# Performance work log

Measured on AMD Instinct MI355X. Metric: run time of the kernel, lower is better.

The kernel has to match this reference:

```python
import jax, jax.numpy as jnp
import numpy as np

KH = KW = 3  # deform conv kernel
EPS = 1e-12  # F.normalize eps


def _deform_sample(img, u, v):
    """Flow-guided deformable sampling: bilinear gather of img at each of the
    9 kernel offsets shifted by the per-pixel flow (u=dx, v=dy).
    img: [B,C,H,W]; u,v: [B,1,H,W] -> returns [B,C,9,H,W]."""
    B, C, H, W = img.shape
    ky, kx = jnp.meshgrid(jnp.arange(KH) - 1, jnp.arange(KW) - 1, indexing='ij')
    ky = ky.reshape(1, 9, 1, 1).astype(img.dtype)
    kx = kx.reshape(1, 9, 1, 1).astype(img.dtype)
    iy = jnp.arange(H, dtype=img.dtype).reshape(1, 1, H, 1)
    ix = jnp.arange(W, dtype=img.dtype).reshape(1, 1, 1, W)
    py = iy + ky + v  # [B,9,H,W]
    px = ix + kx + u
    y0 = jnp.floor(py); x0 = jnp.floor(px)
    wy = py - y0; wx = px - x0  # bilinear weights
    y0i = y0.astype(jnp.int32); x0i = x0.astype(jnp.int32)
    flat = img.reshape(B, C, H * W)

    def gather(yi, xi):
        valid = ((yi >= 0) & (yi < H) & (xi >= 0) & (xi < W)).astype(img.dtype)
        idx = jnp.clip(yi, 0, H - 1) * W + jnp.clip(xi, 0, W - 1)  # [B,9,H,W]
        g = jax.vmap(lambda f, i: jnp.take(f, i.reshape(-1), axis=1))(flat, idx)
        return g.reshape(B, C, 9, H, W) * valid[:, None]

    s = (gather(y0i, x0i) * ((1 - wy) * (1 - wx))[:, None]
         + gather(y0i, x0i + 1) * ((1 - wy) * wx)[:, None]
         + gather(y0i + 1, x0i) * (wy * (1 - wx))[:, None]
         + gather(y0i + 1, x0i + 1) * (wy * wx)[:, None])
    return s


def setup_inputs() -> dict:
    key = jax.random.key(0)
    k1, k2, k3, k4, k5 = jax.random.split(key, 5)
    B, C, H, W = 2, 64, 256, 256
    num_heads = 4
    clone = jax.random.normal(k1, (B, C, H, W), dtype=jnp.float32)
    x = jax.random.normal(k2, (B, C, H * W), dtype=jnp.float32)
    u = jax.random.normal(k3, (B, 1, H, W), dtype=jnp.float32)
    v = jax.random.normal(k4, (B, 1, H, W), dtype=jnp.float32)
    weight = jax.random.normal(k5, (C, C, KH, KW), dtype=jnp.float32) * 0.05
    temperature = jnp.ones((num_heads, 1, 1), dtype=jnp.float32)
    return {"clone": clone, "x": x, "u": u, "v": v,
            "weight": weight, "temperature": temperature}


def reference(clone, x, u, v, weight, temperature):
    # deformable conv: bilinear gather then contract over (in_ch, kernel)
    s = _deform_sample(clone, u, v)                      # [B,C,9,H,W]
    w = weight.reshape(weight.shape[0], weight.shape[1], 9)
    conv = jnp.einsum('bckhw,ock->bohw', s, w)           # [B,C,H,W]
    B, C, H, W = conv.shape
    head = temperature.shape[0]
    kv = conv.reshape(B, head, C // head, H * W)          # k = v = deform output
    q = x.reshape(B, head, C // head, H * W)
    qn = q / jnp.maximum(jnp.linalg.norm(q, axis=-1, keepdims=True), EPS)
    kn = kv / jnp.maximum(jnp.linalg.norm(kv, axis=-1, keepdims=True), EPS)
    attn = jnp.einsum('bhcs,bhds->bhcd', qn, kn) * temperature  # [B,h,c,c]
    attn = jax.nn.softmax(attn, axis=-1)
    out = jnp.einsum('bhcd,bhds->bhcs', attn, kv)
    return out.reshape(B, C, H * W)
```

## Files before the change

### kernel.cpp

```cpp
#include <hip/hip_runtime.h>

typedef __bf16 bf16;
typedef __bf16 bf16x4 __attribute__((ext_vector_type(4)));
typedef __bf16 bf16x8 __attribute__((ext_vector_type(8)));
typedef float  f32x2  __attribute__((ext_vector_type(2)));
typedef float  f32x4  __attribute__((ext_vector_type(4)));
typedef float  f32x16 __attribute__((ext_vector_type(16)));

#define HH 256
#define WW 256
#define NB 2
#define NC 64
#define NS 65536
#define EX 258
#define NHEAD 4
#define DH 16
#define NSTRIPE 8
#define ACCSZ 2304

#define OFF_CEXT   0ul
#define OFF_KV     17040384ul
#define OFF_WPK    33817600ul
#define OFF_ACC    33891328ul

__global__ void k0w(const float* __restrict__ wgt, bf16* __restrict__ wpk,
                    float* __restrict__ accums) {
    int t = blockIdx.x * 256 + threadIdx.x;
    if (t < 9 * 2 * 4 * 64) {
        int L   = t & 63;
        int mtg = (t >> 6) & 3;
        int kc  = (t >> 8) & 1;
        int tap = t >> 9;
        int o  = mtg * 16 + (L & 15);
        int cb = kc * 32 + (L >> 4) * 8;
        bf16x8 vv;
        #pragma unroll
        for (int j = 0; j < 8; j++)
            vv[j] = (bf16)wgt[(o * 64 + (cb + j)) * 9 + tap];
        *(bf16x8*)(wpk + t * 8) = vv;
    }
    int z = t - 9 * 2 * 4 * 64;
    if (z >= 0 && z < NSTRIPE * ACCSZ) accums[z] = 0.0f;
}

__global__ __launch_bounds__(256, 2) void k1_conv(const float* __restrict__ clone,
                                                  const bf16* __restrict__ wpk,
                                                  bf16* __restrict__ cext) {
    const int Xt = blockIdx.x;
    const int Yt = blockIdx.y;
    const int b  = blockIdx.z;
    const int t  = threadIdx.x;
    const int L  = t & 63;
    const int wv = t >> 6;
    const int mpair = wv >> 1;
    const int npair = wv & 1;

    extern __shared__ bf16 tile[];

    bf16x8 afrag[2][9][2];
    #pragma unroll
    for (int mt = 0; mt < 2; mt++)
        #pragma unroll
        for (int tap = 0; tap < 9; tap++)
            #pragma unroll
            for (int kc = 0; kc < 2; kc++) {
                int idx = ((tap * 2 + kc) * 4 + (mpair * 2 + mt)) * 64 + L;
                afrag[mt][tap][kc] = *(const bf16x8*)(wpk + idx * 8);
            }

    for (int u = t; u < 2176; u += 256) {
        int xq = u % 17;
        int rc = u / 17;
        int cg = rc & 15;
        int r  = rc >> 4;
        int y  = Yt * 6 - 2 + r;
        int xg0 = Xt * 64 - 4 + xq * 4;
        int c0 = cg * 4;
        f32x4 f[4];
        bool yin = (y >= 0) && (y < HH);
        if (yin && xg0 >= 0 && xg0 + 3 < WW) {
            #pragma unroll
            for (int i = 0; i < 4; i++)
                f[i] = *(const f32x4*)(clone + ((size_t)(b * NC + c0 + i) * HH + y) * WW + xg0);
        } else {
            #pragma unroll
            for (int i = 0; i < 4; i++)
                #pragma unroll
                for (int e = 0; e < 4; e++) {
                    int xg = xg0 + e;
                    f[i][e] = (yin && xg >= 0 && xg < WW)
                            ? clone[((size_t)(b * NC + c0 + i) * HH + y) * WW + xg] : 0.0f;
                }
        }
        #pragma unroll
        for (int e = 0; e < 4; e++) {
            bf16x4 h;
            #pragma unroll
            for (int i = 0; i < 4; i++) h[i] = (bf16)f[i][e];
            *(bf16x4*)(tile + (r * 68 + xq * 4 + e) * 72 + c0) = h;
        }
    }
    __syncthreads();

    const int nbase = Xt * 64 + npair * 32;
    const f32x4 zero4 = {0.0f, 0.0f, 0.0f, 0.0f};
    for (int Yi = 0; Yi < 6; Yi++) {
        f32x4 acc[2][2];
        acc[0][0] = zero4; acc[0][1] = zero4; acc[1][0] = zero4; acc[1][1] = zero4;
        #pragma unroll
        for (int tap = 0; tap < 9; tap++) {
            const int ky = tap / 3 - 1;
            const int kx = tap % 3 - 1;
            const int r = Yi + 1 + ky;
            #pragma unroll
            for (int kc = 0; kc < 2; kc++) {
                const int cb = kc * 32 + (L >> 4) * 8;
                #pragma unroll
                for (int nt = 0; nt < 2; nt++) {
                    if (nbase + nt * 16 < EX) {
                        const int col = npair * 32 + nt * 16 + (L & 15) + kx + 3;
                        bf16x8 bfrag = *(const bf16x8*)(tile + (r * 68 + col) * 72 + cb);
                        #pragma unroll
                        for (int mt = 0; mt < 2; mt++)
                            acc[mt][nt] = __builtin_amdgcn_mfma_f32_16x16x32_bf16(
                                afrag[mt][tap][kc], bfrag, acc[mt][nt], 0, 0, 0);
                    }
                }
            }
        }
        int Yp = Yt * 6 + Yi;
        #pragma unroll
        for (int mt = 0; mt < 2; mt++)
            #pragma unroll
            for (int nt = 0; nt < 2; nt++) {
                int Xp = Xt * 64 + npair * 32 + nt * 16 + (L & 15);
                if (Xp < EX) {
                    int o = mpair * 32 + mt * 16 + (L >> 4) * 4;
                    bf16x4 st;
                    #pragma unroll
                    for (int rg = 0; rg < 4; rg++) st[rg] = (bf16)acc[mt][nt][rg];
                    *(bf16x4*)(cext + ((((size_t)b * EX + Yp) * EX + Xp) << 6) + o) = st;
                }
            }
    }
}

__global__ __launch_bounds__(256) void k2_gd(const float* __restrict__ uu,
                                             const float* __restrict__ vv,
                                             const float* __restrict__ x,
                                             const bf16* __restrict__ cext,
                                             bf16* __restrict__ kvT,
                                             float* __restrict__ accums) {
    const int bx = blockIdx.x;
    const int b  = blockIdx.z;
    const int strip = (bx & 7) * 128 + (bx >> 3);
    const int t = threadIdx.x;
    const int px = t >> 2;
    const int q4 = t & 3;
    const int hw = strip * 64 + px;
    const int idx = b * NS + hw;
    const int hy = hw >> 8;
    const int wx = hw & 255;

    __shared__ bf16 tile[64][68];

    float fv = vv[idx];
    float fu = uu[idx];
    float py_f = (float)hy + fv;
    float px_f = (float)wx + fu;
    float fy = floorf(py_f);
    float fx = floorf(px_f);
    float ay = py_f - fy;
    float ax = px_f - fx;
    int ys = (int)fy + 1;
    int xs = (int)fx + 1;
    float w00 = (1.0f - ay) * (1.0f - ax);
    float w01 = (1.0f - ay) * ax;
    float w10 = ay * (1.0f - ax);
    float w11 = ay * ax;
    bool y0i = (ys >= 0) && (ys < EX);
    bool y1i = (ys + 1 >= 0) && (ys + 1 < EX);
    bool x0i = (xs >= 0) && (xs < EX);
    bool x1i = (xs + 1 >= 0) && (xs + 1 < EX);
    if (!y0i) { w00 = 0.0f; w01 = 0.0f; }
    if (!y1i) { w10 = 0.0f; w11 = 0.0f; }
    if (!x0i) { w00 = 0.0f; w10 = 0.0f; }
    if (!x1i) { w01 = 0.0f; w11 = 0.0f; }
    int y0c = ys < 0 ? 0 : (ys > EX - 1 ? EX - 1 : ys);
    int y1c = ys + 1 < 0 ? 0 : (ys + 1 > EX - 1 ? EX - 1 : ys + 1);
    int x0c = xs < 0 ? 0 : (xs > EX - 1 ? EX - 1 : xs);
    int x1c = xs + 1 < 0 ? 0 : (xs + 1 > EX - 1 ? EX - 1 : xs + 1);
    const bf16* pb = cext + (((size_t)b * EX * EX) << 6);
    size_t i00 = ((size_t)(y0c * EX + x0c)) << 6;
    size_t i01 = ((size_t)(y0c * EX + x1c)) << 6;
    size_t i10 = ((size_t)(y1c * EX + x0c)) << 6;
    size_t i11 = ((size_t)(y1c * EX + x1c)) << 6;
    const int c0 = q4 * 16;
    bf16* kvp = kvT + ((size_t)(b * NS + hw)) * 64 + c0;
    #pragma unroll
    for (int g = 0; g < 2; g++) {
        int cg = c0 + g * 8;
        bf16x8 c00 = *(const bf16x8*)(pb + i00 + cg);
        bf16x8 c01 = *(const bf16x8*)(pb + i01 + cg);
        bf16x8 c10 = *(const bf16x8*)(pb + i10 + cg);
        bf16x8 c11 = *(const bf16x8*)(pb + i11 + cg);
        bf16x4 lo, hi;
        bf16x8 sv;
        #pragma unroll
        for (int j = 0; j < 8; j++) {
            float val = w00 * (float)c00[j] + w01 * (float)c01[j]
                      + w10 * (float)c10[j] + w11 * (float)c11[j];
            bf16 hv = (bf16)val;
            sv[j] = hv;
            if (j < 4) lo[j] = hv; else hi[j - 4] = hv;
        }
        *(bf16x8*)(kvp + g * 8) = sv;
        *(bf16x4*)(&tile[px][cg])     = lo;
        *(bf16x4*)(&tile[px][cg + 4]) = hi;
    }
    __syncthreads();

    const int L  = t & 63;
    const int h  = t >> 6;
    const int row = L & 15;
    const int kg  = L >> 4;
    const int bh = b * NHEAD + h;
    const float* qb = x + ((size_t)(b * NC + h * DH + row)) * NS + strip * 64;
    f32x4 acc = {0.0f, 0.0f, 0.0f, 0.0f};
    float qp = 0.0f, kp = 0.0f;
    #pragma unroll
    for (int it = 0; it < 2; it++) {
        const int s = it * 32 + kg * 8;
        f32x4 q0 = *(const f32x4*)(qb + s);
        f32x4 q1 = *(const f32x4*)(qb + s + 4);
        bf16x8 qa, ka;
        #pragma unroll
        for (int j = 0; j < 4; j++) {
            qa[j]     = (bf16)q0[j];
            qa[j + 4] = (bf16)q1[j];
        }
        #pragma unroll
        for (int j = 0; j < 8; j++) ka[j] = tile[s + j][h * DH + row];
        qp += q0[0]*q0[0] + q0[1]*q0[1] + q0[2]*q0[2] + q0[3]*q0[3]
            + q1[0]*q1[0] + q1[1]*q1[1] + q1[2]*q1[2] + q1[3]*q1[3];
        #pragma unroll
        for (int j = 0; j < 8; j++) {
            float kf = (float)ka[j];
            kp += kf * kf;
        }
        acc = __builtin_amdgcn_mfma_f32_16x16x32_bf16(qa, ka, acc, 0, 0, 0);
    }
    float* astripe = accums + (bx & 7) * ACCSZ;
    #pragma unroll
    for (int rg = 0; rg < 4; rg++)
        atomicAdd(astripe + bh * 256 + (kg * 4 + rg) * 16 + row, acc[rg]);
    qp += __shfl_xor(qp, 16); qp += __shfl_xor(qp, 32);
    kp += __shfl_xor(kp, 16); kp += __shfl_xor(kp, 32);
    if (kg == 0) {
        atomicAdd(astripe + 2048 + bh * 16 + row, qp);
        atomicAdd(astripe + 2176 + bh * 16 + row, kp);
    }
}

__global__ __launch_bounds__(256) void k5_out(const bf16* __restrict__ kvT,
                                              const float* __restrict__ accums,
                                              const float* __restrict__ temp,
                                              float* __restrict__ out) {
    const int bx = blockIdx.x;
    const int ci = (bx & 7) * 16 + (bx >> 3);
    const int h  = blockIdx.y;
    const int b  = blockIdx.z;
    const int t  = threadIdx.x;
    const int bh = b * NHEAD + h;
    __shared__ float l[256];
    __shared__ float a[256];
    {
        int i = t >> 4, j = t & 15;
        float dsum = 0.0f, q2 = 0.0f, k2 = 0.0f;
        #pragma unroll
        for (int st = 0; st < NSTRIPE; st++) {
            dsum += accums[st * ACCSZ + bh * 256 + t];
            q2   += accums[st * ACCSZ + 2048 + bh * 16 + i];
            k2   += accums[st * ACCSZ + 2176 + bh * 16 + j];
        }
        float qn = fmaxf(sqrtf(q2), 1e-12f);
        float kn = fmaxf(sqrtf(k2), 1e-12f);
        float logit = dsum / (qn * kn) * temp[h];
        l[t] = logit;
        __syncthreads();
        float mx = -1e30f;
        #pragma unroll
        for (int jj = 0; jj < 16; jj++) mx = fmaxf(mx, l[i * 16 + jj]);
        float sum = 0.0f;
        #pragma unroll
        for (int jj = 0; jj < 16; jj++) sum += expf(l[i * 16 + jj] - mx);
        a[t] = expf(logit - mx) / sum;
        __syncthreads();
    }

    const int L   = t & 63;
    const int wv  = t >> 6;
    const int r31 = L & 31;
    const int h5  = L >> 5;

    bf16x8 af;
    #pragma unroll
    for (int j = 0; j < 8; j++) {
        if (r31 < 16) {
            af[j] = (bf16)a[r31 * 16 + h5 * 8 + j];
        } else {
            float v  = a[(r31 - 16) * 16 + h5 * 8 + j];
            bf16 hv = (bf16)v;
            af[j] = (bf16)(v - (float)hv);
        }
    }

    const bf16* kvb = kvT + ((size_t)b * NS) * 64 + h * DH + h5 * 8;
    #pragma unroll
    for (int ch = 0; ch < 4; ch++) {
        const int s0 = ci * 512 + wv * 128 + ch * 32;
        bf16x8 kb = *(const bf16x8*)(kvb + (size_t)(s0 + r31) * 64);
        f32x16 acc;
        #pragma unroll
        for (int z = 0; z < 16; z++) acc[z] = 0.0f;
        acc = __builtin_amdgcn_mfma_f32_32x32x16_bf16(af, kb, acc, 0, 0, 0);
        #pragma unroll
        for (int reg = 0; reg < 8; reg++) {
            const int orow = (reg & 3) + 8 * (reg >> 2) + 4 * h5;
            out[(((size_t)(b * NC + h * DH + orow)) << 16) + s0 + r31]
                = acc[reg] + acc[reg + 8];
        }
    }
}

extern "C" void kernel_launch(void* const* d_in, const int* in_sizes, int n_in,
                              void* d_out, int out_size, void* d_ws, size_t ws_size,
                              hipStream_t stream) {
    const float* clone = (const float*)d_in[0];
    const float* x     = (const float*)d_in[1];
    const float* u     = (const float*)d_in[2];
    const float* v     = (const float*)d_in[3];
    const float* wgt   = (const float*)d_in[4];
    const float* temp  = (const float*)d_in[5];
    float* out = (float*)d_out;

    char* ws = (char*)d_ws;
    bf16*  cext   = (bf16*) (ws + OFF_CEXT);
    bf16*  kvT    = (bf16*) (ws + OFF_KV);
    bf16*  wpk    = (bf16*) (ws + OFF_WPK);
    float* accums = (float*)(ws + OFF_ACC);

    static bool attr_set = false;
    if (!attr_set) {
        hipFuncSetAttribute((const void*)k1_conv,
                            hipFuncAttributeMaxDynamicSharedMemorySize, 78336);
        attr_set = true;
    }

    k0w<<<90, 256, 0, stream>>>(wgt, wpk, accums);
    k1_conv<<<dim3(5, 43, 2), 256, 78336, stream>>>(clone, wpk, cext);
    k2_gd<<<dim3(1024, 1, 2), 256, 0, stream>>>(u, v, x, cext, kvT, accums);
    k5_out<<<dim3(128, 4, 2), 256, 0, stream>>>(kvT, accums, temp, out);
}
```

Before: 156.6 us.

## Stage conv-output window in shared memory for deformable gather

The gather kernel now processes 32-pixel strips and first loads a 9x40-pixel, 64-channel window of the conv output into LDS cooperatively. Bilinear corner reads are then served from LDS, with a fallback to global memory when the flow displaces a sample outside the window. This targets scattered, redundant global reads of neighbouring pixels. In exchange it adds about 46KB of LDS per block, doubles the grid with half the MFMA work per block, and issues twice as many accumulator atomics.

```diff
diff --git a/kernel.cpp b/kernel.cpp
--- a/kernel.cpp
+++ b/kernel.cpp
@@ -145,6 +145,8 @@
     }
 }
 
+#define WR 9
+#define WC 40
 __global__ __launch_bounds__(256) void k2_gd(const float* __restrict__ uu,
                                              const float* __restrict__ vv,
                                              const float* __restrict__ x,
@@ -153,57 +155,75 @@
                                              float* __restrict__ accums) {
     const int bx = blockIdx.x;
     const int b  = blockIdx.z;
-    const int strip = (bx & 7) * 128 + (bx >> 3);
+    const int strip = (bx & 7) * 256 + (bx >> 3);
     const int t = threadIdx.x;
-    const int px = t >> 2;
-    const int q4 = t & 3;
-    const int hw = strip * 64 + px;
-    const int idx = b * NS + hw;
-    const int hy = hw >> 8;
-    const int wx = hw & 255;
-
-    __shared__ bf16 tile[64][68];
-
-    float fv = vv[idx];
-    float fu = uu[idx];
-    float py_f = (float)hy + fv;
-    float px_f = (float)wx + fu;
-    float fy = floorf(py_f);
-    float fx = floorf(px_f);
-    float ay = py_f - fy;
-    float ax = px_f - fx;
-    int ys = (int)fy + 1;
-    int xs = (int)fx + 1;
-    float w00 = (1.0f - ay) * (1.0f - ax);
-    float w01 = (1.0f - ay) * ax;
-    float w10 = ay * (1.0f - ax);
-    float w11 = ay * ax;
-    bool y0i = (ys >= 0) && (ys < EX);
-    bool y1i = (ys + 1 >= 0) && (ys + 1 < EX);
-    bool x0i = (xs >= 0) && (xs < EX);
-    bool x1i = (xs + 1 >= 0) && (xs + 1 < EX);
-    if (!y0i) { w00 = 0.0f; w01 = 0.0f; }
-    if (!y1i) { w10 = 0.0f; w11 = 0.0f; }
-    if (!x0i) { w00 = 0.0f; w10 = 0.0f; }
-    if (!x1i) { w01 = 0.0f; w11 = 0.0f; }
-    int y0c = ys < 0 ? 0 : (ys > EX - 1 ? EX - 1 : ys);
-    int y1c = ys + 1 < 0 ? 0 : (ys + 1 > EX - 1 ? EX - 1 : ys + 1);
-    int x0c = xs < 0 ? 0 : (xs > EX - 1 ? EX - 1 : xs);
-    int x1c = xs + 1 < 0 ? 0 : (xs + 1 > EX - 1 ? EX - 1 : xs + 1);
+    const int y  = strip >> 3;
+    const int xb = (strip & 7) * 32;
+
+    __shared__ bf16 stage[WR * WC * 64];
+    __shared__ bf16 tile[32][68];
+
     const bf16* pb = cext + (((size_t)b * EX * EX) << 6);
-    size_t i00 = ((size_t)(y0c * EX + x0c)) << 6;
-    size_t i01 = ((size_t)(y0c * EX + x1c)) << 6;
-    size_t i10 = ((size_t)(y1c * EX + x0c)) << 6;
-    size_t i11 = ((size_t)(y1c * EX + x1c)) << 6;
-    const int c0 = q4 * 16;
-    bf16* kvp = kvT + ((size_t)(b * NS + hw)) * 64 + c0;
-    #pragma unroll
-    for (int g = 0; g < 2; g++) {
-        int cg = c0 + g * 8;
-        bf16x8 c00 = *(const bf16x8*)(pb + i00 + cg);
-        bf16x8 c01 = *(const bf16x8*)(pb + i01 + cg);
-        bf16x8 c10 = *(const bf16x8*)(pb + i10 + cg);
-        bf16x8 c11 = *(const bf16x8*)(pb + i11 + cg);
+
+    for (int u = t; u < WR * WC * 8; u += 256) {
+        int p  = u & 7;
+        int li = u >> 3;
+        int wr = li / WC;
+        int wc = li - wr * WC;
+        int gr = y - 3 + wr;  gr = gr < 0 ? 0 : (gr > EX - 1 ? EX - 1 : gr);
+        int gc = xb - 3 + wc; gc = gc < 0 ? 0 : (gc > EX - 1 ? EX - 1 : gc);
+        *(bf16x8*)(stage + li * 64 + p * 8) =
+            *(const bf16x8*)(pb + (((size_t)(gr * EX + gc)) << 6) + p * 8);
+    }
+    __syncthreads();
+
+    {
+        const int px = t >> 3;
+        const int c0 = (t & 7) * 8;
+        const int hw = strip * 32 + px;
+        const int idx = b * NS + hw;
+        const int wx = xb + px;
+        float fv = vv[idx];
+        float fu = uu[idx];
+        float py_f = (float)y + fv;
+        float px_f = (float)wx + fu;
+        float fy = floorf(py_f);
+        float fx = floorf(px_f);
+        float ay = py_f - fy;
+        float ax = px_f - fx;
+        int ys = (int)fy + 1;
+        int xs = (int)fx + 1;
+        float w00 = (1.0f - ay) * (1.0f - ax);
+        float w01 = (1.0f - ay) * ax;
+        float w10 = ay * (1.0f - ax);
+        float w11 = ay * ax;
+        bool y0i = (ys >= 0) && (ys < EX);
+        bool y1i = (ys + 1 >= 0) && (ys + 1 < EX);
+        bool x0i = (xs >= 0) && (xs < EX);
+        bool x1i = (xs + 1 >= 0) && (xs + 1 < EX);
+        if (!y0i) { w00 = 0.0f; w01 = 0.0f; }
+        if (!y1i) { w10 = 0.0f; w11 = 0.0f; }
+        if (!x0i) { w00 = 0.0f; w10 = 0.0f; }
+        if (!x1i) { w01 = 0.0f; w11 = 0.0f; }
+        int y0c = ys < 0 ? 0 : (ys > EX - 1 ? EX - 1 : ys);
+        int y1c = ys + 1 < 0 ? 0 : (ys + 1 > EX - 1 ? EX - 1 : ys + 1);
+        int x0c = xs < 0 ? 0 : (xs > EX - 1 ? EX - 1 : xs);
+        int x1c = xs + 1 < 0 ? 0 : (xs + 1 > EX - 1 ? EX - 1 : xs + 1);
+        int ry0 = y0c - (y - 3), ry1 = y1c - (y - 3);
+        int cx0 = x0c - (xb - 3), cx1 = x1c - (xb - 3);
+        bf16x8 c00, c01, c10, c11;
+        if ((unsigned)ry0 < WR && (unsigned)ry1 < WR &&
+            (unsigned)cx0 < WC && (unsigned)cx1 < WC) {
+            c00 = *(const bf16x8*)(stage + (ry0 * WC + cx0) * 64 + c0);
+            c01 = *(const bf16x8*)(stage + (ry0 * WC + cx1) * 64 + c0);
+            c10 = *(const bf16x8*)(stage + (ry1 * WC + cx0) * 64 + c0);
+            c11 = *(const bf16x8*)(stage + (ry1 * WC + cx1) * 64 + c0);
+        } else {
+            c00 = *(const bf16x8*)(pb + (((size_t)(y0c * EX + x0c)) << 6) + c0);
+            c01 = *(const bf16x8*)(pb + (((size_t)(y0c * EX + x1c)) << 6) + c0);
+            c10 = *(const bf16x8*)(pb + (((size_t)(y1c * EX + x0c)) << 6) + c0);
+            c11 = *(const bf16x8*)(pb + (((size_t)(y1c * EX + x1c)) << 6) + c0);
+        }
         bf16x4 lo, hi;
         bf16x8 sv;
         #pragma unroll
@@ -214,9 +234,9 @@
             sv[j] = hv;
             if (j < 4) lo[j] = hv; else hi[j - 4] = hv;
         }
-        *(bf16x8*)(kvp + g * 8) = sv;
-        *(bf16x4*)(&tile[px][cg])     = lo;
-        *(bf16x4*)(&tile[px][cg + 4]) = hi;
+        *(bf16x8*)(kvT + ((size_t)(b * NS + hw)) * 64 + c0) = sv;
+        *(bf16x4*)(&tile[px][c0])     = lo;
+        *(bf16x4*)(&tile[px][c0 + 4]) = hi;
     }
     __syncthreads();
 
@@ -225,31 +245,29 @@
     const int row = L & 15;
     const int kg  = L >> 4;
     const int bh = b * NHEAD + h;
-    const float* qb = x + ((size_t)(b * NC + h * DH + row)) * NS + strip * 64;
+    const float* qb = x + ((size_t)(b * NC + h * DH + row)) * NS + strip * 32;
+    const int s = kg * 8;
+    f32x4 q0 = *(const f32x4*)(qb + s);
+    f32x4 q1 = *(const f32x4*)(qb + s + 4);
+    bf16x8 qa, ka;
+    #pragma unroll
+    for (int j = 0; j < 4; j++) {
+        qa[j]     = (bf16)q0[j];
+        qa[j + 4] = (bf16)q1[j];
+    }
+    #pragma unroll
+    for (int j = 0; j < 8; j++) ka[j] = tile[s + j][h * DH + row];
+    float qp = q0[0]*q0[0] + q0[1]*q0[1] + q0[2]*q0[2] + q0[3]*q0[3]
+             + q1[0]*q1[0] + q1[1]*q1[1] + q1[2]*q1[2] + q1[3]*q1[3];
+    float kp = 0.0f;
+    #pragma unroll
+    for (int j = 0; j < 8; j++) {
+        float kf = (float)ka[j];
+        kp += kf * kf;
+    }
     f32x4 acc = {0.0f, 0.0f, 0.0f, 0.0f};
-    float qp = 0.0f, kp = 0.0f;
-    #pragma unroll
-    for (int it = 0; it < 2; it++) {
-        const int s = it * 32 + kg * 8;
-        f32x4 q0 = *(const f32x4*)(qb + s);
-        f32x4 q1 = *(const f32x4*)(qb + s + 4);
-        bf16x8 qa, ka;
-        #pragma unroll
-        for (int j = 0; j < 4; j++) {
-            qa[j]     = (bf16)q0[j];
-            qa[j + 4] = (bf16)q1[j];
-        }
-        #pragma unroll
-        for (int j = 0; j < 8; j++) ka[j] = tile[s + j][h * DH + row];
-        qp += q0[0]*q0[0] + q0[1]*q0[1] + q0[2]*q0[2] + q0[3]*q0[3]
-            + q1[0]*q1[0] + q1[1]*q1[1] + q1[2]*q1[2] + q1[3]*q1[3];
-        #pragma unroll
-        for (int j = 0; j < 8; j++) {
-            float kf = (float)ka[j];
-            kp += kf * kf;
-        }
-        acc = __builtin_amdgcn_mfma_f32_16x16x32_bf16(qa, ka, acc, 0, 0, 0);
-    }
+    acc = __builtin_amdgcn_mfma_f32_16x16x32_bf16(qa, ka, acc, 0, 0, 0);
+
     float* astripe = accums + (bx & 7) * ACCSZ;
     #pragma unroll
     for (int rg = 0; rg < 4; rg++)
@@ -359,6 +377,6 @@
 
     k0w<<<90, 256, 0, stream>>>(wgt, wpk, accums);
     k1_conv<<<dim3(5, 43, 2), 256, 78336, stream>>>(clone, wpk, cext);
-    k2_gd<<<dim3(1024, 1, 2), 256, 0, stream>>>(u, v, x, cext, kvT, accums);
+    k2_gd<<<dim3(2048, 1, 2), 256, 0, stream>>>(u, v, x, cext, kvT, accums);
     k5_out<<<dim3(128, 4, 2), 256, 0, stream>>>(kvT, accums, temp, out);
 }
```

Result: slower. 175.9 us (+12.3%).
